# Kernel optimization log

Measured on AMD Instinct MI355X. Metric: run time of the kernel, lower is better.

The kernel has to match this reference:

```python
import jax, jax.numpy as jnp
import numpy as np

B_, L_, D_MODEL, N_LAYER, VOCAB = 4, 2048, 512, 2, 128
D_INNER, D_STATE, DT_RANK, D_CONV = 2 * D_MODEL, 16, D_MODEL // 16, 4
NDIR = 2  # forward / backward Mamba stacks


def setup_inputs() -> dict:
    key = jax.random.key(0)
    ks = jax.random.split(key, 12)
    f = jax.random.normal
    A_init = jnp.broadcast_to(
        jnp.log(jnp.arange(1, D_STATE + 1, dtype=jnp.float32)),
        (NDIR, N_LAYER, D_INNER, D_STATE)) + 0.0
    return {
        "input_ids": jax.random.randint(ks[0], (B_, L_), 0, VOCAB),
        "padding_mask": jnp.ones((B_, L_), dtype=bool),
        "embed": 0.02 * f(ks[1], (NDIR, VOCAB, D_MODEL)),
        "in_proj_w": 0.02 * f(ks[2], (NDIR, N_LAYER, 2 * D_INNER, D_MODEL)),
        "conv_w": 0.1 * f(ks[3], (NDIR, N_LAYER, D_INNER, 1, D_CONV)),
        "conv_b": 0.1 * f(ks[4], (NDIR, N_LAYER, D_INNER)),
        "x_proj_w": 0.02 * f(ks[5], (NDIR, N_LAYER, DT_RANK + 2 * D_STATE, D_INNER)),
        "dt_proj_w": 0.1 * f(ks[6], (NDIR, N_LAYER, D_INNER, DT_RANK)),
        "dt_proj_b": -4.0 + 0.5 * jax.random.uniform(ks[7], (NDIR, N_LAYER, D_INNER)),
        "A_log": A_init,
        "D": jnp.ones((NDIR, N_LAYER, D_INNER)),
        "out_proj_w": 0.02 * f(ks[8], (NDIR, N_LAYER, D_MODEL, D_INNER)),
        "norm_w": jnp.ones((NDIR, N_LAYER, D_MODEL)),
        "norm_f_w": jnp.ones((NDIR, D_MODEL)),
        "proj_w": 0.02 * f(ks[9], (D_MODEL, 2 * D_MODEL)),
        "proj_b": jnp.zeros((D_MODEL,)),
    }


def _rmsnorm(x, w, eps=1e-5):
    return x * jax.lax.rsqrt(jnp.mean(jnp.square(x), axis=-1, keepdims=True) + eps) * w


def _selective_scan(u, dt, Bm, Cm, A, Dp):
    # u, dt: (b, l, d_inner); Bm, Cm: (b, l, d_state)
    b, l, di = u.shape

    def step(h, inp):
        u_t, dt_t, b_t, c_t = inp                      # (b,di) (b,di) (b,n) (b,n)
        dA = jnp.exp(dt_t[:, :, None] * A)             # (b, di, n)
        h = dA * h + (dt_t * u_t)[:, :, None] * b_t[:, None, :]
        return h, jnp.einsum('bdn,bn->bd', h, c_t)

    h0 = jnp.zeros((b, di, A.shape[-1]), u.dtype)
    xs = (jnp.swapaxes(u, 0, 1), jnp.swapaxes(dt, 0, 1),
          jnp.swapaxes(Bm, 0, 1), jnp.swapaxes(Cm, 0, 1))
    _, ys = jax.lax.scan(step, h0, xs)                 # ys: (l, b, di)
    return jnp.swapaxes(ys, 0, 1) + u * Dp


def _mamba(x, p):
    in_w, cw, cb, xw, dtw, dtb, alog, dp, ow = p
    xz = jnp.einsum('bld,ed->ble', x, in_w)            # (b, l, 2*d_inner)
    u, z = jnp.split(xz, 2, axis=-1)
    uc = jnp.swapaxes(u, 1, 2)                         # (b, d_inner, l)
    uc = jax.lax.conv_general_dilated(
        uc, cw, (1,), [(D_CONV - 1, 0)], feature_group_count=D_INNER)
    u = jax.nn.silu(jnp.swapaxes(uc + cb[None, :, None], 1, 2))
    xdbl = jnp.einsum('bld,ed->ble', u, xw)
    dt, Bm, Cm = jnp.split(xdbl, [DT_RANK, DT_RANK + D_STATE], axis=-1)
    dt = jax.nn.softplus(jnp.einsum('blr,dr->bld', dt, dtw) + dtb)
    y = _selective_scan(u, dt, Bm, Cm, -jnp.exp(alog), dp)
    y = y * jax.nn.silu(z)
    return jnp.einsum('bld,ed->ble', y, ow)


def _mixer(ids, d, embed, in_proj_w, conv_w, conv_b, x_proj_w, dt_proj_w,
           dt_proj_b, A_log, D, out_proj_w, norm_w, norm_f_w):
    hidden = embed[d][ids]
    residual = None
    for i in range(N_LAYER):
        residual = hidden if residual is None else hidden + residual
        hidden = _rmsnorm(residual, norm_w[d, i])
        p = (in_proj_w[d, i], conv_w[d, i], conv_b[d, i], x_proj_w[d, i],
             dt_proj_w[d, i], dt_proj_b[d, i], A_log[d, i], D[d, i],
             out_proj_w[d, i])
        hidden = _mamba(hidden, p)
    return _rmsnorm(hidden + residual, norm_f_w[d])


def reference(input_ids, padding_mask, embed, in_proj_w, conv_w, conv_b,
              x_proj_w, dt_proj_w, dt_proj_b, A_log, D, out_proj_w, norm_w,
              norm_f_w, proj_w, proj_b):
    args = (embed, in_proj_w, conv_w, conv_b, x_proj_w, dt_proj_w, dt_proj_b,
            A_log, D, out_proj_w, norm_w, norm_f_w)
    fwd = _mixer(input_ids, 0, *args)
    bwd = jnp.flip(_mixer(jnp.flip(input_ids, 1), 1, *args), 1)
    out = jnp.concatenate([fwd, bwd], axis=-1)        # (b, l, 2*d_model)
    return jnp.einsum('ble,oe->blo', out, proj_w) + proj_b
```

## Files before the change

### kernel.cpp

```cpp
#include <hip/hip_runtime.h>
#include <hip/hip_bf16.h>

#define B_   4
#define L_   2048
#define DM   512
#define DI   1024
#define NST  16
#define DTR  32
#define ROWS  (B_ * L_)
#define ROWS2 (2 * ROWS)
#define NCHUNK 32
#define CLEN  (L_ / NCHUNK)
#define LN2R 1.4426950408889634f

typedef unsigned short u16;
typedef __attribute__((ext_vector_type(8))) short bf16x8;
typedef __attribute__((ext_vector_type(4))) float f32x4;
typedef __attribute__((ext_vector_type(4))) float float4v;
typedef __attribute__((ext_vector_type(2))) float f32x2;

__device__ __forceinline__ float bf2f(u16 h) {
  union { unsigned int u; float f; } v; v.u = ((unsigned int)h) << 16; return v.f;
}
__device__ __forceinline__ u16 f2bf(float f) {
  union { float f; unsigned int u; } v; v.f = f;
  unsigned int u = v.u;
  if ((u & 0x7fffffffu) > 0x7f800000u) return (u16)((u >> 16) | 0x0040u);
  return (u16)((u + 0x7fffu + ((u >> 16) & 1u)) >> 16);
}
__device__ __forceinline__ float sigmoidf_(float x) { return 1.f / (1.f + __expf(-x)); }

__device__ __forceinline__ f32x2 pk_mul(f32x2 a, f32x2 b) {
  f32x2 d; asm("v_pk_mul_f32 %0, %1, %2" : "=v"(d) : "v"(a), "v"(b)); return d;
}
__device__ __forceinline__ f32x2 pk_fma(f32x2 a, f32x2 b, f32x2 c) {
  f32x2 d; asm("v_pk_fma_f32 %0, %1, %2, %3" : "=v"(d) : "v"(a), "v"(b), "v"(c)); return d;
}

__device__ __forceinline__ void gload16(const u16* g, u16* l) {
  __builtin_amdgcn_global_load_lds(
      (const __attribute__((address_space(1))) void*)g,
      (__attribute__((address_space(3))) void*)l, 16, 0, 0);
}

__global__ __launch_bounds__(256) void cvt_k(const float* __restrict__ in,
                                             u16* __restrict__ out, int n4) {
  int i = blockIdx.x * 256 + threadIdx.x;
  if (i >= n4) return;
  float4v v = *(const float4v*)&in[i * 4];
  u16 o[4];
  o[0] = f2bf(v.x); o[1] = f2bf(v.y); o[2] = f2bf(v.z); o[3] = f2bf(v.w);
  *(ulong1*)&out[i * 4] = *(ulong1*)o;
}

__global__ __launch_bounds__(256) void trp_k(const float* __restrict__ in,
                                             float* __restrict__ out) {
  int o = blockIdx.x * 256 + threadIdx.x;
  int li = o >> 15;
  int k = (o >> 10) & (DTR - 1);
  int d = o & (DI - 1);
  out[o] = in[((size_t)li * DI + d) * DTR + k];
}

__global__ __launch_bounds__(256) void embed_k(const int* __restrict__ ids,
                                               const float* __restrict__ emb,
                                               float* __restrict__ res) {
  int idx = blockIdx.x * 256 + threadIdx.x;
  int c = idx & (DM - 1);
  int row = idx >> 9;
  int dir = row >> 13;
  int r = row & (ROWS - 1);
  int b = r >> 11;
  int l = r & (L_ - 1);
  int sl = dir ? (L_ - 1 - l) : l;
  int id = ids[(b << 11) + sl];
  res[idx] = emb[(size_t)dir * 128 * DM + id * DM + c];
}

template <bool ADD>
__global__ __launch_bounds__(256) void addnorm_k(float* __restrict__ res,
                                                 const float* __restrict__ hid,
                                                 const float* __restrict__ norm_w,
                                                 int layer,
                                                 u16* __restrict__ xn) {
  int row = blockIdx.x;
  int dir = row >> 13;
  const float* w = norm_w + (size_t)(dir * 2 + layer) * DM;
  int tid = threadIdx.x;
  int base = row * DM;
  float x0 = res[base + tid];
  float x1 = res[base + 256 + tid];
  if (ADD) {
    x0 += hid[base + tid];
    x1 += hid[base + 256 + tid];
    res[base + tid] = x0;
    res[base + 256 + tid] = x1;
  }
  float s = x0 * x0 + x1 * x1;
  for (int off = 32; off; off >>= 1) s += __shfl_xor(s, off);
  __shared__ float ps[4];
  if (!(tid & 63)) ps[tid >> 6] = s;
  __syncthreads();
  float tot = ps[0] + ps[1] + ps[2] + ps[3];
  float rs = 1.f / sqrtf(tot / (float)DM + 1e-5f);
  xn[base + tid]       = f2bf(x0 * rs * w[tid]);
  xn[base + 256 + tid] = f2bf(x1 * rs * w[tid + 256]);
}

#define MFMA_B16(a, b, c) __builtin_amdgcn_mfma_f32_16x16x32_bf16(a, b, c, 0, 0, 0)

__global__ __launch_bounds__(512) void gemm8p_k(const u16* __restrict__ A,
                                                const u16* __restrict__ W,
                                                u16* __restrict__ outU,
                                                u16* __restrict__ outZ,
                                                int K) {
  __shared__ u16 As[2][2][256 * 32];
  __shared__ u16 Wsh[2][2][256 * 32];
  int tid = threadIdx.x;
  int lane = tid & 63;
  int wv = tid >> 6;
  int wr = wv >> 2, wc = wv & 3;
  int bid = blockIdx.x;
  int xcd = bid & 7, jj = bid >> 3;
  int mt = xcd * 8 + (jj & 7);
  int nt = jj >> 3;
  int m0 = mt * 256, n0 = nt * 256;
  const u16* Weff = W + (size_t)(m0 >> 13) * (size_t)2 * (2 * DI) * DM;
  f32x4 acc[8][4];
#pragma unroll
  for (int i = 0; i < 8; ++i)
#pragma unroll
    for (int j = 0; j < 4; ++j) acc[i][j] = (f32x4){0.f, 0.f, 0.f, 0.f};
  int rr = lane & 15;
  int sl = lane >> 4;
  int pofs = ((sl + (rr >> 1)) & 3) * 8;
  int lr = lane >> 2;
  int ls = ((lane & 3) - (lr >> 1)) & 3;

  auto stA = [&](int tau, int ks) {
    int buf = tau & 1;
#pragma unroll
    for (int j = 0; j < 2; ++j)
      gload16(A + (size_t)(m0 + j * 128 + wv * 16 + lr) * K + tau * 64 + ks * 32 + ls * 8,
              &As[buf][ks][(j * 128 + wv * 16) * 32]);
  };
  auto stW = [&](int tau, int ks) {
    int buf = tau & 1;
#pragma unroll
    for (int j = 0; j < 2; ++j)
      gload16(Weff + (size_t)(n0 + j * 128 + wv * 16 + lr) * K + tau * 64 + ks * 32 + ls * 8,
              &Wsh[buf][ks][(j * 128 + wv * 16) * 32]);
  };

  int NT = K / 64;
  stA(0, 0); stW(0, 0); stA(0, 1); stW(0, 1);
  asm volatile("s_waitcnt vmcnt(4)" ::: "memory");
  __builtin_amdgcn_sched_barrier(0);
  __builtin_amdgcn_s_barrier();
  __builtin_amdgcn_sched_barrier(0);

  for (int tau = 0; tau < NT; ++tau) {
    int buf = tau & 1;
    bool more = (tau + 1 < NT);
    bf16x8 af[8], w0, w1;
#pragma unroll
    for (int mi = 0; mi < 8; ++mi)
      af[mi] = *(bf16x8*)&As[buf][0][(wr * 128 + mi * 16 + rr) * 32 + pofs];
    w0 = *(bf16x8*)&Wsh[buf][0][(wc * 64 + 0 * 16 + rr) * 32 + pofs];
    w1 = *(bf16x8*)&Wsh[buf][0][(wc * 64 + 1 * 16 + rr) * 32 + pofs];
    if (more) stA(tau + 1, 0);
    __builtin_amdgcn_sched_barrier(0);
    __builtin_amdgcn_s_barrier();
    asm volatile("s_waitcnt lgkmcnt(0)" ::: "memory");
    __builtin_amdgcn_sched_barrier(0);
    __builtin_amdgcn_s_setprio(1);
#pragma unroll
    for (int mi = 0; mi < 8; ++mi) {
      acc[mi][0] = MFMA_B16(af[mi], w0, acc[mi][0]);
      acc[mi][1] = MFMA_B16(af[mi], w1, acc[mi][1]);
    }
    __builtin_amdgcn_s_setprio(0);
    __builtin_amdgcn_s_barrier();
    __builtin_amdgcn_sched_barrier(0);
    w0 = *(bf16x8*)&Wsh[buf][0][(wc * 64 + 2 * 16 + rr) * 32 + pofs];
    w1 = *(bf16x8*)&Wsh[buf][0][(wc * 64 + 3 * 16 + rr) * 32 + pofs];
    if (more) {
      stW(tau + 1, 0);
      asm volatile("s_waitcnt vmcnt(4)" ::: "memory");
    } else {
      asm volatile("s_waitcnt vmcnt(0)" ::: "memory");
    }
    __builtin_amdgcn_sched_barrier(0);
    __builtin_amdgcn_s_barrier();
    asm volatile("s_waitcnt lgkmcnt(0)" ::: "memory");
    __builtin_amdgcn_sched_barrier(0);
    __builtin_amdgcn_s_setprio(1);
#pragma unroll
    for (int mi = 0; mi < 8; ++mi) {
      acc[mi][2] = MFMA_B16(af[mi], w0, acc[mi][2]);
      acc[mi][3] = MFMA_B16(af[mi], w1, acc[mi][3]);
    }
    __builtin_amdgcn_s_setprio(0);
    __builtin_amdgcn_s_barrier();
    __builtin_amdgcn_sched_barrier(0);
#pragma unroll
    for (int mi = 0; mi < 8; ++mi)
      af[mi] = *(bf16x8*)&As[buf][1][(wr * 128 + mi * 16 + rr) * 32 + pofs];
    w0 = *(bf16x8*)&Wsh[buf][1][(wc * 64 + 0 * 16 + rr) * 32 + pofs];
    w1 = *(bf16x8*)&Wsh[buf][1][(wc * 64 + 1 * 16 + rr) * 32 + pofs];
    if (more) stA(tau + 1, 1);
    __builtin_amdgcn_sched_barrier(0);
    __builtin_amdgcn_s_barrier();
    asm volatile("s_waitcnt lgkmcnt(0)" ::: "memory");
    __builtin_amdgcn_sched_barrier(0);
    __builtin_amdgcn_s_setprio(1);
#pragma unroll
    for (int mi = 0; mi < 8; ++mi) {
      acc[mi][0] = MFMA_B16(af[mi], w0, acc[mi][0]);
      acc[mi][1] = MFMA_B16(af[mi], w1, acc[mi][1]);
    }
    __builtin_amdgcn_s_setprio(0);
    __builtin_amdgcn_s_barrier();
    __builtin_amdgcn_sched_barrier(0);
    w0 = *(bf16x8*)&Wsh[buf][1][(wc * 64 + 2 * 16 + rr) * 32 + pofs];
    w1 = *(bf16x8*)&Wsh[buf][1][(wc * 64 + 3 * 16 + rr) * 32 + pofs];
    if (more) {
      stW(tau + 1, 1);
      asm volatile("s_waitcnt vmcnt(4)" ::: "memory");
    }
    __builtin_amdgcn_sched_barrier(0);
    __builtin_amdgcn_s_barrier();
    asm volatile("s_waitcnt lgkmcnt(0)" ::: "memory");
    __builtin_amdgcn_sched_barrier(0);
    __builtin_amdgcn_s_setprio(1);
#pragma unroll
    for (int mi = 0; mi < 8; ++mi) {
      acc[mi][2] = MFMA_B16(af[mi], w0, acc[mi][2]);
      acc[mi][3] = MFMA_B16(af[mi], w1, acc[mi][3]);
    }
    __builtin_amdgcn_s_setprio(0);
    __builtin_amdgcn_s_barrier();
    __builtin_amdgcn_sched_barrier(0);
  }
  int cr = (lane >> 4) << 2;
  int cc = lane & 15;
  u16* outp = (n0 < DI) ? outU : outZ;
  int cb0 = (n0 < DI) ? n0 : (n0 - DI);
#pragma unroll
  for (int mi = 0; mi < 8; ++mi)
#pragma unroll
    for (int ni = 0; ni < 4; ++ni) {
      int row = m0 + wr * 128 + mi * 16 + cr;
      int col = cb0 + wc * 64 + ni * 16 + cc;
#pragma unroll
      for (int j = 0; j < 4; ++j)
        outp[(size_t)(row + j) * DI + col] = f2bf(acc[mi][ni][j]);
    }
}

#define EPI_F32  0
#define EPI_BF16 1
#define EPI_BIAS 2

template <int BN, int EPI, int SK = 1>
__global__ __launch_bounds__(256) void gemm_bt(const u16* __restrict__ A,
                                               const u16* __restrict__ W,
                                               void* __restrict__ outp,
                                               const float* __restrict__ bias,
                                               int N, int K, size_t wsd) {
  constexpr int BM = 128, BK = 32;
  constexpr int NF = BN / 32;
  constexpr int G = (BN == 128) ? 4 : 3;
  __shared__ u16 As[4][BM * BK];
  __shared__ u16 Wsh[4][BN * BK];
  int tid = threadIdx.x;
  int lane = tid & 63;
  int wv = tid >> 6;
  int wr = wv >> 1, wc = wv & 1;
  int m0 = blockIdx.x * BM;
  int n0 = (SK > 1) ? 0 : blockIdx.y * BN;
  int koff = (SK > 1) ? blockIdx.y * (K / SK) : 0;
  int KS = K / SK;
  int NK = KS / BK;
  const u16* Weff = W + (size_t)(m0 >> 13) * wsd;
  f32x4 acc[4][NF];
#pragma unroll
  for (int i = 0; i < 4; ++i)
#pragma unroll
    for (int j = 0; j < NF; ++j) acc[i][j] = (f32x4){0.f, 0.f, 0.f, 0.f};
  int rr = lane & 15;
  int kk = (lane >> 4) << 3;
  int l4 = lane >> 2;
  int c8 = (lane & 3) << 3;
  const u16* Ag = A + (size_t)(m0 + l4) * K + koff + c8;
  const u16* Wg = Weff + (size_t)(n0 + l4) * K + koff + c8;

  auto stage = [&](int k0, int buf) {
    gload16(Ag + (size_t)(wv * 16) * K + k0, &As[buf][wv * 512]);
    gload16(Ag + (size_t)((wv + 4) * 16) * K + k0, &As[buf][(wv + 4) * 512]);
    gload16(Wg + (size_t)(wv * 16) * K + k0, &Wsh[buf][wv * 512]);
    if (BN == 128)
      gload16(Wg + (size_t)((wv + 4) * 16) * K + k0, &Wsh[buf][(wv + 4) * 512]);
  };

  stage(0, 0); stage(BK, 1); stage(2 * BK, 2);
  for (int k = 0; k < NK; ++k) {
    if (k < NK - 2)
      asm volatile("s_waitcnt vmcnt(%0)" :: "n"(2 * G) : "memory");
    else if (k == NK - 2)
      asm volatile("s_waitcnt vmcnt(%0)" :: "n"(G) : "memory");
    else
      asm volatile("s_waitcnt vmcnt(0)" ::: "memory");
    __builtin_amdgcn_s_barrier();
    __builtin_amdgcn_sched_barrier(0);
    if (k + 3 < NK) stage((k + 3) * BK, (k + 3) & 3);
    __builtin_amdgcn_sched_barrier(0);
    int cur = k & 3;
    bf16x8 af[4], wf[NF];
#pragma unroll
    for (int mi = 0; mi < 4; ++mi)
      af[mi] = *(bf16x8*)&As[cur][(wr * 64 + mi * 16 + rr) * BK + kk];
#pragma unroll
    for (int ni = 0; ni < NF; ++ni)
      wf[ni] = *(bf16x8*)&Wsh[cur][(wc * (BN / 2) + ni * 16 + rr) * BK + kk];
#pragma unroll
    for (int mi = 0; mi < 4; ++mi)
#pragma unroll
      for (int ni = 0; ni < NF; ++ni)
        acc[mi][ni] = __builtin_amdgcn_mfma_f32_16x16x32_bf16(af[mi], wf[ni], acc[mi][ni], 0, 0, 0);
  }
  int cr = (lane >> 4) << 2;
  int cc = lane & 15;
  float* outF = (float*)outp +
      ((SK > 1) ? (size_t)blockIdx.y * (size_t)gridDim.x * BM * N : 0);
#pragma unroll
  for (int mi = 0; mi < 4; ++mi)
#pragma unroll
    for (int ni = 0; ni < NF; ++ni) {
      int row = m0 + wr * 64 + mi * 16 + cr;
      int col = n0 + wc * (BN / 2) + ni * 16 + cc;
      float bv = (EPI == EPI_BIAS) ? bias[col] : 0.f;
#pragma unroll
      for (int j = 0; j < 4; ++j) {
        float v = acc[mi][ni][j] + bv;
        if (EPI == EPI_BF16)
          ((u16*)outp)[(size_t)(row + j) * N + col] = f2bf(v);
        else
          outF[(size_t)(row + j) * N + col] = v;
      }
    }
}

__global__ __launch_bounds__(256) void conv_k(const u16* __restrict__ xzu,
                                              const float* __restrict__ conv_w,
                                              const float* __restrict__ conv_b,
                                              int layer,
                                              u16* __restrict__ uh) {
  int idx = blockIdx.x * 256 + threadIdx.x;
  int c = idx & (DI - 1);
  int row = idx >> 10;
  int dir = row >> 13;
  int l = row & (L_ - 1);
  const float* cw = conv_w + (size_t)(dir * 2 + layer) * DI * 4;
  const float* cb = conv_b + (size_t)(dir * 2 + layer) * DI;
  float acc = cb[c];
#pragma unroll
  for (int j = 0; j < 4; ++j) {
    int ls = l + j - 3;
    if (ls >= 0)
      acc += bf2f(xzu[(size_t)(row + j - 3) * DI + c]) * cw[c * 4 + j];
  }
  float s = acc * sigmoidf_(acc);
  uh[idx] = f2bf(s);
}

__device__ __forceinline__ bool a_fast(const float* alog, int d, float& a20) {
  a20 = -__expf(alog[d * NST]) * LN2R;
  bool fast = true;
#pragma unroll
  for (int n = 1; n < NST; ++n) {
    float an = -__expf(alog[d * NST + n]) * LN2R;
    fast &= (fabsf(an - (float)(n + 1) * a20) <= 1e-5f * (float)(n + 1) * fabsf(a20));
  }
  return fast;
}

__device__ __forceinline__ void stage_xs(float (*xs)[64], const float* xp,
                                         size_t rowbase, int tid) {
  size_t base = rowbase * 64;
  const float4v* s0 = (const float4v*)(xp + base);
  const float4v* s1 = (const float4v*)(xp + (size_t)ROWS2 * 64 + base);
  const float4v* s2 = (const float4v*)(xp + (size_t)2 * ROWS2 * 64 + base);
  const float4v* s3 = (const float4v*)(xp + (size_t)3 * ROWS2 * 64 + base);
  float4v* dst = (float4v*)&xs[0][0];
#pragma unroll
  for (int i = 0; i < CLEN / 16; ++i)
    dst[tid + i * 256] = s0[tid + i * 256] + s1[tid + i * 256] +
                         s2[tid + i * 256] + s3[tid + i * 256];
}

__device__ __forceinline__ float dt_of(const float (*xs)[64], int t,
                                       const f32x2* w2, float bias) {
  f32x2 a2 = {bias, 0.f};
  const f32x2* xr2 = (const f32x2*)&xs[t][0];
#pragma unroll
  for (int j = 0; j < 16; ++j) a2 = pk_fma(xr2[j], w2[j], a2);
  float a = a2.x + a2.y;
  return (a > 15.f) ? a : __logf(1.f + __expf(a));
}

__global__ __launch_bounds__(256) void dtscan1_k(const u16* __restrict__ uh,
                                                 const float* __restrict__ xp,
                                                 const float* __restrict__ dtw_t,
                                                 const float* __restrict__ dtb,
                                                 const float* __restrict__ alog_,
                                                 int layer,
                                                 float* __restrict__ chk) {
  __shared__ float xs[CLEN][64];
  int blk = blockIdx.x;
  int db = blk & 3;
  int c  = (blk >> 2) & (NCHUNK - 1);
  int nb = blk >> 7;
  int dir = nb >> 2;
  int tid = threadIdx.x;
  int d  = db * 256 + tid;
  int li = dir * 2 + layer;
  const float* dtwT = dtw_t + (size_t)li * DTR * DI;
  const float* alog = alog_ + (size_t)li * DI * NST;
  int t0 = c * CLEN;
  size_t rowbase = (size_t)nb * L_ + t0;
  stage_xs(xs, xp, rowbase, tid);
  f32x2 w2[16];
#pragma unroll
  for (int j = 0; j < 16; ++j)
    w2[j] = (f32x2){dtwT[(size_t)(2 * j) * DI + d], dtwT[(size_t)(2 * j + 1) * DI + d]};
  float bias = dtb[(size_t)li * DI + d];
  float a20;
  bool fast = a_fast(alog, d, a20);
  __syncthreads();
  float S = 0.f;
  size_t ubase = rowbase * DI + d;
  f32x2 h2[8];
#pragma unroll
  for (int q = 0; q < 8; ++q) h2[q] = (f32x2){0.f, 0.f};
  for (int t = 0; t < CLEN; ++t) {
    float dtv = dt_of(xs, t, w2, bias);
    float du = dtv * bf2f(uh[ubase]);
    S += dtv;
    if (fast) {
      float p1 = exp2f(dtv * a20);
      float p2 = p1 * p1;
      f32x2 pw = {p1, p2};
      f32x2 pst = {p2, p2};
      f32x2 du2 = {du, du};
#pragma unroll
      for (int k = 0; k < 4; ++k) {
        f32x4 bv = *(const f32x4*)&xs[t][DTR + k * 4];
        f32x2 blo = __builtin_shufflevector(bv, bv, 0, 1);
        f32x2 bhi = __builtin_shufflevector(bv, bv, 2, 3);
        h2[2 * k]     = pk_fma(pw, h2[2 * k], pk_mul(du2, blo));
        pw = pk_mul(pw, pst);
        h2[2 * k + 1] = pk_fma(pw, h2[2 * k + 1], pk_mul(du2, bhi));
        if (k < 3) pw = pk_mul(pw, pst);
      }
    } else {
#pragma unroll
      for (int q = 0; q < 8; ++q) {
        float e0 = exp2f(dtv * -__expf(alog[d * NST + 2 * q]) * LN2R);
        float e1 = exp2f(dtv * -__expf(alog[d * NST + 2 * q + 1]) * LN2R);
        f32x2 bv = *(const f32x2*)&xs[t][DTR + q * 2];
        h2[q] = pk_fma((f32x2){e0, e1}, h2[q], pk_mul((f32x2){du, du}, bv));
      }
    }
    ubase += DI;
  }
  const size_t H = (size_t)8 * NCHUNK * DI * NST;
  size_t idx = ((size_t)(nb * NCHUNK + c) * DI + d) * NST;
#pragma unroll
  for (int n = 0; n < NST; ++n) {
    float an = -__expf(alog[d * NST + n]) * LN2R;
    chk[idx + n]     = exp2f(an * S);
    chk[H + idx + n] = (n & 1) ? h2[n >> 1].y : h2[n >> 1].x;
  }
}

__global__ __launch_bounds__(256) void scan2_k(float* __restrict__ chk) {
  int j = blockIdx.x * 256 + threadIdx.x;
  int n = j & 15;
  int d = (j >> 4) & (DI - 1);
  int nb = j >> 14;
  const size_t H = (size_t)8 * NCHUNK * DI * NST;
  float h = 0.f;
  for (int c = 0; c < NCHUNK; ++c) {
    size_t idx = ((size_t)(nb * NCHUNK + c) * DI + d) * NST + n;
    float a = chk[idx];
    float hl = chk[H + idx];
    chk[H + idx] = h;
    h = a * h + hl;
  }
}

__global__ __launch_bounds__(256) void scan3_k(const u16* __restrict__ uh,
                                               const float* __restrict__ xp,
                                               const float* __restrict__ dtw_t,
                                               const float* __restrict__ dtb,
                                               const float* __restrict__ alog_,
                                               const float* __restrict__ Dp,
                                               int layer,
                                               const float* __restrict__ chk,
                                               const u16* __restrict__ xzz,
                                               u16* __restrict__ yg) {
  __shared__ float xs[CLEN][64];
  int blk = blockIdx.x;
  int db = blk & 3;
  int c  = (blk >> 2) & (NCHUNK - 1);
  int nb = blk >> 7;
  int dir = nb >> 2;
  int tid = threadIdx.x;
  int d  = db * 256 + tid;
  int li = dir * 2 + layer;
  const float* dtwT = dtw_t + (size_t)li * DTR * DI;
  const float* alog = alog_ + (size_t)li * DI * NST;
  int t0 = c * CLEN;
  size_t rowbase = (size_t)nb * L_ + t0;
  stage_xs(xs, xp, rowbase, tid);
  f32x2 w2[16];
#pragma unroll
  for (int j = 0; j < 16; ++j)
    w2[j] = (f32x2){dtwT[(size_t)(2 * j) * DI + d], dtwT[(size_t)(2 * j + 1) * DI + d]};
  float bias = dtb[(size_t)li * DI + d];
  float a20;
  bool fast = a_fast(alog, d, a20);
  const size_t H = (size_t)8 * NCHUNK * DI * NST;
  size_t cidx = ((size_t)(nb * NCHUNK + c) * DI + d) * NST;
  f32x2 h2[8];
#pragma unroll
  for (int q = 0; q < 8; ++q) h2[q] = *(const f32x2*)&chk[H + cidx + 2 * q];
  float Dv = Dp[(size_t)li * DI + d];
  __syncthreads();
  size_t ubase = rowbase * DI + d;
  if (fast) {
    for (int t = 0; t < CLEN; ++t) {
      float dtv = dt_of(xs, t, w2, bias);
      float uv  = bf2f(uh[ubase]);
      float du  = dtv * uv;
      float p1 = exp2f(dtv * a20);
      float p2 = p1 * p1;
      f32x2 pw = {p1, p2};
      f32x2 pst = {p2, p2};
      f32x2 du2 = {du, du};
      f32x2 acc2 = {0.f, 0.f};
#pragma unroll
      for (int k = 0; k < 4; ++k) {
        f32x4 bv = *(const f32x4*)&xs[t][DTR + k * 4];
        f32x4 cv = *(const f32x4*)&xs[t][DTR + NST + k * 4];
        f32x2 blo = __builtin_shufflevector(bv, bv, 0, 1);
        f32x2 bhi = __builtin_shufflevector(bv, bv, 2, 3);
        f32x2 clo = __builtin_shufflevector(cv, cv, 0, 1);
        f32x2 chi = __builtin_shufflevector(cv, cv, 2, 3);
        h2[2 * k]     = pk_fma(pw, h2[2 * k], pk_mul(du2, blo));
        acc2          = pk_fma(h2[2 * k], clo, acc2);
        pw = pk_mul(pw, pst);
        h2[2 * k + 1] = pk_fma(pw, h2[2 * k + 1], pk_mul(du2, bhi));
        acc2          = pk_fma(h2[2 * k + 1], chi, acc2);
        if (k < 3) pw = pk_mul(pw, pst);
      }
      float y = acc2.x + acc2.y + uv * Dv;
      float z = bf2f(xzz[ubase]);
      yg[ubase] = f2bf(y * z * sigmoidf_(z));
      ubase += DI;
    }
  } else {
    float A2[NST];
#pragma unroll
    for (int n = 0; n < NST; ++n) A2[n] = -__expf(alog[d * NST + n]) * LN2R;
    for (int t = 0; t < CLEN; ++t) {
      float dtv = dt_of(xs, t, w2, bias);
      float uv  = bf2f(uh[ubase]);
      float du  = dtv * uv;
      f32x2 acc2 = {0.f, 0.f};
#pragma unroll
      for (int q = 0; q < 8; ++q) {
        f32x2 bv = *(const f32x2*)&xs[t][DTR + q * 2];
        f32x2 cv = *(const f32x2*)&xs[t][DTR + NST + q * 2];
        f32x2 e = {exp2f(dtv * A2[2 * q]), exp2f(dtv * A2[2 * q + 1])};
        h2[q] = pk_fma(e, h2[q], pk_mul((f32x2){du, du}, bv));
        acc2 = pk_fma(h2[q], cv, acc2);
      }
      float y = acc2.x + acc2.y + uv * Dv;
      float z = bf2f(xzz[ubase]);
      yg[ubase] = f2bf(y * z * sigmoidf_(z));
      ubase += DI;
    }
  }
}

__global__ __launch_bounds__(256) void fincat_k(const float* __restrict__ hid,
                                                const float* __restrict__ res,
                                                const float* __restrict__ norm_f,
                                                u16* __restrict__ cat) {
  int row = blockIdx.x;
  int dir = row >> 13;
  const float* w = norm_f + (size_t)dir * DM;
  int tid = threadIdx.x;
  int base = row * DM;
  float x0 = hid[base + tid] + res[base + tid];
  float x1 = hid[base + 256 + tid] + res[base + 256 + tid];
  float s = x0 * x0 + x1 * x1;
  for (int off = 32; off; off >>= 1) s += __shfl_xor(s, off);
  __shared__ float ps[4];
  if (!(tid & 63)) ps[tid >> 6] = s;
  __syncthreads();
  float tot = ps[0] + ps[1] + ps[2] + ps[3];
  float rs = 1.f / sqrtf(tot / (float)DM + 1e-5f);
  int r = row & (ROWS - 1);
  int b = r >> 11, l = r & (L_ - 1);
  size_t drow = dir ? ((size_t)(b << 11) + (L_ - 1 - l)) : (size_t)r;
  size_t obase = drow * (2 * DM) + (size_t)dir * DM;
  cat[obase + tid]       = f2bf(x0 * rs * w[tid]);
  cat[obase + 256 + tid] = f2bf(x1 * rs * w[tid + 256]);
}

extern "C" void kernel_launch(void* const* d_in, const int* in_sizes, int n_in,
                              void* d_out, int out_size, void* d_ws, size_t ws_size,
                              hipStream_t stream) {
  const int*   ids      = (const int*)d_in[0];
  const float* embed    = (const float*)d_in[2];
  const float* in_w     = (const float*)d_in[3];
  const float* conv_w   = (const float*)d_in[4];
  const float* conv_b   = (const float*)d_in[5];
  const float* x_w      = (const float*)d_in[6];
  const float* dt_w     = (const float*)d_in[7];
  const float* dt_bias  = (const float*)d_in[8];
  const float* A_log    = (const float*)d_in[9];
  const float* Dp       = (const float*)d_in[10];
  const float* out_w    = (const float*)d_in[11];
  const float* norm_w   = (const float*)d_in[12];
  const float* norm_f   = (const float*)d_in[13];
  const float* proj_w   = (const float*)d_in[14];
  const float* proj_b   = (const float*)d_in[15];

  char* ws = (char*)d_ws;
  size_t off = 0;
  auto alloc = [&](size_t bytes) {
    void* p = ws + off;
    off += (bytes + 255) & ~(size_t)255;
    return p;
  };
  float* res  = (float*)alloc((size_t)ROWS2 * DM * 4);
  float* hid  = (float*)alloc((size_t)ROWS2 * DM * 4);
  u16*   xnyg = (u16*)alloc((size_t)ROWS2 * DI * 2);
  u16*   xzz  = (u16*)alloc((size_t)ROWS2 * DI * 2);
  void*  shrd = alloc((size_t)ROWS2 * DI * 2);
  u16*   u_h  = (u16*)alloc((size_t)ROWS2 * DI * 2);
  const int N_IN  = 4 * 2 * DI * DM;
  const int N_XW  = 4 * 64 * DI;
  const int N_OW  = 4 * DM * DI;
  const int N_PW  = DM * 2 * DM;
  const int N_DTW = 4 * DTR * DI;
  u16*   in_wb  = (u16*)alloc((size_t)N_IN * 2);
  u16*   x_wb   = (u16*)alloc((size_t)N_XW * 2);
  u16*   out_wb = (u16*)alloc((size_t)N_OW * 2);
  u16*   pr_wb  = (u16*)alloc((size_t)N_PW * 2);
  float* dtw_t  = (float*)alloc((size_t)N_DTW * 4);
  if (off > ws_size) return;

  u16*   xzu = (u16*)shrd;
  float* chk = (float*)shrd;
  u16*   cat = (u16*)shrd;

  cvt_k<<<(N_IN / 4 + 255) / 256, 256, 0, stream>>>(in_w, in_wb, N_IN / 4);
  cvt_k<<<(N_XW / 4 + 255) / 256, 256, 0, stream>>>(x_w, x_wb, N_XW / 4);
  cvt_k<<<(N_OW / 4 + 255) / 256, 256, 0, stream>>>(out_w, out_wb, N_OW / 4);
  cvt_k<<<(N_PW / 4 + 255) / 256, 256, 0, stream>>>(proj_w, pr_wb, N_PW / 4);
  trp_k<<<N_DTW / 256, 256, 0, stream>>>(dt_w, dtw_t);

  embed_k<<<ROWS2 * DM / 256, 256, 0, stream>>>(ids, embed, res);
  for (int i = 0; i < 2; ++i) {
    if (i == 0)
      addnorm_k<false><<<ROWS2, 256, 0, stream>>>(res, hid, norm_w, i, xnyg);
    else
      addnorm_k<true><<<ROWS2, 256, 0, stream>>>(res, hid, norm_w, i, xnyg);
    gemm8p_k<<<512, 512, 0, stream>>>(
        xnyg, in_wb + (size_t)i * 2 * DI * DM, xzu, xzz, DM);
    conv_k<<<ROWS2 * DI / 256, 256, 0, stream>>>(xzu, conv_w, conv_b, i, u_h);
    gemm_bt<64, EPI_F32, 4><<<dim3(ROWS2 / 128, 4), 256, 0, stream>>>(
        u_h, x_wb + (size_t)i * 64 * DI, hid, nullptr, 64, DI, (size_t)2 * 64 * DI);
    dtscan1_k<<<1024, 256, 0, stream>>>(u_h, hid, dtw_t, dt_bias, A_log, i, chk);
    scan2_k<<<512, 256, 0, stream>>>(chk);
    scan3_k<<<1024, 256, 0, stream>>>(u_h, hid, dtw_t, dt_bias, A_log, Dp, i,
                                      chk, xzz, xnyg);
    gemm_bt<64, EPI_F32><<<dim3(ROWS2 / 128, DM / 64), 256, 0, stream>>>(
        xnyg, out_wb + (size_t)i * DM * DI, hid, nullptr, DM, DI, (size_t)2 * DM * DI);
  }
  fincat_k<<<ROWS2, 256, 0, stream>>>(hid, res, norm_f, cat);
  gemm_bt<64, EPI_BIAS><<<dim3(ROWS / 128, DM / 64), 256, 0, stream>>>(
      cat, pr_wb, (float*)d_out, proj_b, DM, DI, 0);
}
```

Baseline: 775.3 us.

## Compute local scan outputs in pass one and apply carry-in correction in light pass three

The first chunked-scan pass now also produces each chunk's local output y (with a zero initial state, plus the D skip term) and the running cumulative dt, writing them over the u buffer and the output buffer in bf16. The third pass no longer recomputes dt, the recurrence and B terms. It only adds the carry-in contribution C·(exp(A·S)·h0) and applies the gating. This removes the duplicated dt projection and recurrence from pass three, at the cost of extra bf16 writes and reads and some precision loss from storing cumulative dt and partial y in bf16.

```diff
diff --git a/kernel.cpp b/kernel.cpp
--- a/kernel.cpp
+++ b/kernel.cpp
@@ -409,12 +409,14 @@
   return (a > 15.f) ? a : __logf(1.f + __expf(a));
 }
 
-__global__ __launch_bounds__(256) void dtscan1_k(const u16* __restrict__ uh,
+__global__ __launch_bounds__(256) void dtscan1_k(u16* uS,
                                                  const float* __restrict__ xp,
                                                  const float* __restrict__ dtw_t,
                                                  const float* __restrict__ dtb,
                                                  const float* __restrict__ alog_,
+                                                 const float* __restrict__ Dp,
                                                  int layer,
+                                                 u16* __restrict__ ylg,
                                                  float* __restrict__ chk) {
   __shared__ float xs[CLEN][64];
   int blk = blockIdx.x;
@@ -435,6 +437,7 @@
   for (int j = 0; j < 16; ++j)
     w2[j] = (f32x2){dtwT[(size_t)(2 * j) * DI + d], dtwT[(size_t)(2 * j + 1) * DI + d]};
   float bias = dtb[(size_t)li * DI + d];
+  float Dv = Dp[(size_t)li * DI + d];
   float a20;
   bool fast = a_fast(alog, d, a20);
   __syncthreads();
@@ -445,111 +448,16 @@
   for (int q = 0; q < 8; ++q) h2[q] = (f32x2){0.f, 0.f};
   for (int t = 0; t < CLEN; ++t) {
     float dtv = dt_of(xs, t, w2, bias);
-    float du = dtv * bf2f(uh[ubase]);
+    float uv = bf2f(uS[ubase]);
+    float du = dtv * uv;
     S += dtv;
+    f32x2 acc2 = {0.f, 0.f};
     if (fast) {
       float p1 = exp2f(dtv * a20);
       float p2 = p1 * p1;
       f32x2 pw = {p1, p2};
       f32x2 pst = {p2, p2};
       f32x2 du2 = {du, du};
-#pragma unroll
-      for (int k = 0; k < 4; ++k) {
-        f32x4 bv = *(const f32x4*)&xs[t][DTR + k * 4];
-        f32x2 blo = __builtin_shufflevector(bv, bv, 0, 1);
-        f32x2 bhi = __builtin_shufflevector(bv, bv, 2, 3);
-        h2[2 * k]     = pk_fma(pw, h2[2 * k], pk_mul(du2, blo));
-        pw = pk_mul(pw, pst);
-        h2[2 * k + 1] = pk_fma(pw, h2[2 * k + 1], pk_mul(du2, bhi));
-        if (k < 3) pw = pk_mul(pw, pst);
-      }
-    } else {
-#pragma unroll
-      for (int q = 0; q < 8; ++q) {
-        float e0 = exp2f(dtv * -__expf(alog[d * NST + 2 * q]) * LN2R);
-        float e1 = exp2f(dtv * -__expf(alog[d * NST + 2 * q + 1]) * LN2R);
-        f32x2 bv = *(const f32x2*)&xs[t][DTR + q * 2];
-        h2[q] = pk_fma((f32x2){e0, e1}, h2[q], pk_mul((f32x2){du, du}, bv));
-      }
-    }
-    ubase += DI;
-  }
-  const size_t H = (size_t)8 * NCHUNK * DI * NST;
-  size_t idx = ((size_t)(nb * NCHUNK + c) * DI + d) * NST;
-#pragma unroll
-  for (int n = 0; n < NST; ++n) {
-    float an = -__expf(alog[d * NST + n]) * LN2R;
-    chk[idx + n]     = exp2f(an * S);
-    chk[H + idx + n] = (n & 1) ? h2[n >> 1].y : h2[n >> 1].x;
-  }
-}
-
-__global__ __launch_bounds__(256) void scan2_k(float* __restrict__ chk) {
-  int j = blockIdx.x * 256 + threadIdx.x;
-  int n = j & 15;
-  int d = (j >> 4) & (DI - 1);
-  int nb = j >> 14;
-  const size_t H = (size_t)8 * NCHUNK * DI * NST;
-  float h = 0.f;
-  for (int c = 0; c < NCHUNK; ++c) {
-    size_t idx = ((size_t)(nb * NCHUNK + c) * DI + d) * NST + n;
-    float a = chk[idx];
-    float hl = chk[H + idx];
-    chk[H + idx] = h;
-    h = a * h + hl;
-  }
-}
-
-__global__ __launch_bounds__(256) void scan3_k(const u16* __restrict__ uh,
-                                               const float* __restrict__ xp,
-                                               const float* __restrict__ dtw_t,
-                                               const float* __restrict__ dtb,
-                                               const float* __restrict__ alog_,
-                                               const float* __restrict__ Dp,
-                                               int layer,
-                                               const float* __restrict__ chk,
-                                               const u16* __restrict__ xzz,
-                                               u16* __restrict__ yg) {
-  __shared__ float xs[CLEN][64];
-  int blk = blockIdx.x;
-  int db = blk & 3;
-  int c  = (blk >> 2) & (NCHUNK - 1);
-  int nb = blk >> 7;
-  int dir = nb >> 2;
-  int tid = threadIdx.x;
-  int d  = db * 256 + tid;
-  int li = dir * 2 + layer;
-  const float* dtwT = dtw_t + (size_t)li * DTR * DI;
-  const float* alog = alog_ + (size_t)li * DI * NST;
-  int t0 = c * CLEN;
-  size_t rowbase = (size_t)nb * L_ + t0;
-  stage_xs(xs, xp, rowbase, tid);
-  f32x2 w2[16];
-#pragma unroll
-  for (int j = 0; j < 16; ++j)
-    w2[j] = (f32x2){dtwT[(size_t)(2 * j) * DI + d], dtwT[(size_t)(2 * j + 1) * DI + d]};
-  float bias = dtb[(size_t)li * DI + d];
-  float a20;
-  bool fast = a_fast(alog, d, a20);
-  const size_t H = (size_t)8 * NCHUNK * DI * NST;
-  size_t cidx = ((size_t)(nb * NCHUNK + c) * DI + d) * NST;
-  f32x2 h2[8];
-#pragma unroll
-  for (int q = 0; q < 8; ++q) h2[q] = *(const f32x2*)&chk[H + cidx + 2 * q];
-  float Dv = Dp[(size_t)li * DI + d];
-  __syncthreads();
-  size_t ubase = rowbase * DI + d;
-  if (fast) {
-    for (int t = 0; t < CLEN; ++t) {
-      float dtv = dt_of(xs, t, w2, bias);
-      float uv  = bf2f(uh[ubase]);
-      float du  = dtv * uv;
-      float p1 = exp2f(dtv * a20);
-      float p2 = p1 * p1;
-      f32x2 pw = {p1, p2};
-      f32x2 pst = {p2, p2};
-      f32x2 du2 = {du, du};
-      f32x2 acc2 = {0.f, 0.f};
 #pragma unroll
       for (int k = 0; k < 4; ++k) {
         f32x4 bv = *(const f32x4*)&xs[t][DTR + k * 4];
@@ -565,33 +473,116 @@
         acc2          = pk_fma(h2[2 * k + 1], chi, acc2);
         if (k < 3) pw = pk_mul(pw, pst);
       }
-      float y = acc2.x + acc2.y + uv * Dv;
-      float z = bf2f(xzz[ubase]);
-      yg[ubase] = f2bf(y * z * sigmoidf_(z));
-      ubase += DI;
-    }
-  } else {
-    float A2[NST];
-#pragma unroll
-    for (int n = 0; n < NST; ++n) A2[n] = -__expf(alog[d * NST + n]) * LN2R;
-    for (int t = 0; t < CLEN; ++t) {
-      float dtv = dt_of(xs, t, w2, bias);
-      float uv  = bf2f(uh[ubase]);
-      float du  = dtv * uv;
-      f32x2 acc2 = {0.f, 0.f};
+    } else {
 #pragma unroll
       for (int q = 0; q < 8; ++q) {
+        float e0 = exp2f(dtv * -__expf(alog[d * NST + 2 * q]) * LN2R);
+        float e1 = exp2f(dtv * -__expf(alog[d * NST + 2 * q + 1]) * LN2R);
         f32x2 bv = *(const f32x2*)&xs[t][DTR + q * 2];
         f32x2 cv = *(const f32x2*)&xs[t][DTR + NST + q * 2];
-        f32x2 e = {exp2f(dtv * A2[2 * q]), exp2f(dtv * A2[2 * q + 1])};
-        h2[q] = pk_fma(e, h2[q], pk_mul((f32x2){du, du}, bv));
+        h2[q] = pk_fma((f32x2){e0, e1}, h2[q], pk_mul((f32x2){du, du}, bv));
         acc2 = pk_fma(h2[q], cv, acc2);
       }
-      float y = acc2.x + acc2.y + uv * Dv;
-      float z = bf2f(xzz[ubase]);
-      yg[ubase] = f2bf(y * z * sigmoidf_(z));
-      ubase += DI;
-    }
+    }
+    float yloc = acc2.x + acc2.y + uv * Dv;
+    ylg[ubase] = f2bf(yloc);
+    uS[ubase]  = f2bf(S);
+    ubase += DI;
+  }
+  const size_t H = (size_t)8 * NCHUNK * DI * NST;
+  size_t idx = ((size_t)(nb * NCHUNK + c) * DI + d) * NST;
+#pragma unroll
+  for (int n = 0; n < NST; ++n) {
+    float an = -__expf(alog[d * NST + n]) * LN2R;
+    chk[idx + n]     = exp2f(an * S);
+    chk[H + idx + n] = (n & 1) ? h2[n >> 1].y : h2[n >> 1].x;
+  }
+}
+
+__global__ __launch_bounds__(256) void scan2_k(float* __restrict__ chk) {
+  int j = blockIdx.x * 256 + threadIdx.x;
+  int n = j & 15;
+  int d = (j >> 4) & (DI - 1);
+  int nb = j >> 14;
+  const size_t H = (size_t)8 * NCHUNK * DI * NST;
+  float h = 0.f;
+  for (int c = 0; c < NCHUNK; ++c) {
+    size_t idx = ((size_t)(nb * NCHUNK + c) * DI + d) * NST + n;
+    float a = chk[idx];
+    float hl = chk[H + idx];
+    chk[H + idx] = h;
+    h = a * h + hl;
+  }
+}
+
+__global__ __launch_bounds__(256) void scan3lite_k(const u16* __restrict__ uS,
+                                                   const float* __restrict__ xp,
+                                                   const float* __restrict__ alog_,
+                                                   int layer,
+                                                   const float* __restrict__ chk,
+                                                   const u16* __restrict__ xzz,
+                                                   u16* ylg) {
+  __shared__ float xc[CLEN][NST];
+  int blk = blockIdx.x;
+  int db = blk & 3;
+  int c  = (blk >> 2) & (NCHUNK - 1);
+  int nb = blk >> 7;
+  int dir = nb >> 2;
+  int tid = threadIdx.x;
+  int d  = db * 256 + tid;
+  int li = dir * 2 + layer;
+  const float* alog = alog_ + (size_t)li * DI * NST;
+  int t0 = c * CLEN;
+  size_t rowbase = (size_t)nb * L_ + t0;
+  {
+    int r = tid >> 2, v = tid & 3;
+    size_t base = (rowbase + r) * 64 + DTR + NST + v * 4;
+    float4v s = *(const float4v*)(xp + base)
+              + *(const float4v*)(xp + (size_t)ROWS2 * 64 + base)
+              + *(const float4v*)(xp + (size_t)2 * ROWS2 * 64 + base)
+              + *(const float4v*)(xp + (size_t)3 * ROWS2 * 64 + base);
+    *(float4v*)&xc[r][v * 4] = s;
+  }
+  float a20;
+  bool fast = a_fast(alog, d, a20);
+  const size_t H = (size_t)8 * NCHUNK * DI * NST;
+  size_t cidx = ((size_t)(nb * NCHUNK + c) * DI + d) * NST;
+  f32x2 h2[8];
+#pragma unroll
+  for (int q = 0; q < 8; ++q) h2[q] = *(const f32x2*)&chk[H + cidx + 2 * q];
+  float A2g[NST];
+  if (!fast) {
+#pragma unroll
+    for (int n = 0; n < NST; ++n) A2g[n] = -__expf(alog[d * NST + n]) * LN2R;
+  }
+  __syncthreads();
+  size_t ubase = rowbase * DI + d;
+  for (int t = 0; t < CLEN; ++t) {
+    float S = bf2f(uS[ubase]);
+    f32x2 corr2 = {0.f, 0.f};
+    if (fast) {
+      float w1 = exp2f(a20 * S);
+      float w2_ = w1 * w1;
+      f32x2 pw = {w1, w2_};
+      f32x2 pst = {w2_, w2_};
+#pragma unroll
+      for (int q = 0; q < 8; ++q) {
+        f32x2 cp = *(const f32x2*)&xc[t][2 * q];
+        corr2 = pk_fma(pk_mul(pw, h2[q]), cp, corr2);
+        if (q < 7) pw = pk_mul(pw, pst);
+      }
+    } else {
+#pragma unroll
+      for (int q = 0; q < 8; ++q) {
+        f32x2 e = {exp2f(A2g[2 * q] * S), exp2f(A2g[2 * q + 1] * S)};
+        f32x2 cp = *(const f32x2*)&xc[t][2 * q];
+        corr2 = pk_fma(pk_mul(e, h2[q]), cp, corr2);
+      }
+    }
+    float y = bf2f(ylg[ubase]) + corr2.x + corr2.y;
+    float z = bf2f(xzz[ubase]);
+    ylg[ubase] = f2bf(y * z * sigmoidf_(z));
+    ubase += DI;
   }
 }
 
@@ -686,10 +677,10 @@
     conv_k<<<ROWS2 * DI / 256, 256, 0, stream>>>(xzu, conv_w, conv_b, i, u_h);
     gemm_bt<64, EPI_F32, 4><<<dim3(ROWS2 / 128, 4), 256, 0, stream>>>(
         u_h, x_wb + (size_t)i * 64 * DI, hid, nullptr, 64, DI, (size_t)2 * 64 * DI);
-    dtscan1_k<<<1024, 256, 0, stream>>>(u_h, hid, dtw_t, dt_bias, A_log, i, chk);
+    dtscan1_k<<<1024, 256, 0, stream>>>(u_h, hid, dtw_t, dt_bias, A_log, Dp, i,
+                                        xnyg, chk);
     scan2_k<<<512, 256, 0, stream>>>(chk);
-    scan3_k<<<1024, 256, 0, stream>>>(u_h, hid, dtw_t, dt_bias, A_log, Dp, i,
-                                      chk, xzz, xnyg);
+    scan3lite_k<<<1024, 256, 0, stream>>>(u_h, hid, A_log, i, chk, xzz, xnyg);
     gemm_bt<64, EPI_F32><<<dim3(ROWS2 / 128, DM / 64), 256, 0, stream>>>(
         xnyg, out_wb + (size_t)i * DM * DI, hid, nullptr, DM, DI, (size_t)2 * DM * DI);
   }
```

Result: no change. 771.1 us (-0.5%).
